# Optimization experiments

Measured on AMD Instinct MI355X. Metric: run time of the kernel, lower is better.

The kernel has to match this reference:

```python
import jax, jax.numpy as jnp
import numpy as np

B, T, C = 4, 2048, 1024
NUM_EXPERTS = 8
TOP_K = 2
D_EXPERT = 4 * C * TOP_K // NUM_EXPERTS  # 1024


def setup_inputs() -> dict:
    key = jax.random.key(0)
    k0, k1, k2, k3 = jax.random.split(key, 4)
    x = jax.random.normal(k0, (B, T, C), dtype=jnp.float32)
    # nn.Linear(n_embd, num_experts, bias=False).weight has shape [E, C]
    router_w = jax.random.normal(k1, (NUM_EXPERTS, C), dtype=jnp.float32) * 0.02
    # w1_all = stack of c_fc.weight.T  -> [E, C, D]
    w1_all = jax.random.normal(k2, (NUM_EXPERTS, C, D_EXPERT), dtype=jnp.float32) * 0.02
    # w2_all = stack of c_proj.weight.T -> [E, D, C]
    w2_all = jax.random.normal(k3, (NUM_EXPERTS, D_EXPERT, C), dtype=jnp.float32) * 0.02
    return {"x": x, "router_w": router_w, "w1_all": w1_all, "w2_all": w2_all}


def reference(x, router_w, w1_all, w2_all):
    b, t, c = x.shape
    x_flat = x.reshape(-1, c)                      # [N, C]
    router_logits = x_flat @ router_w.T            # [N, E]
    top_k_logits, top_k_idx = jax.lax.top_k(router_logits, TOP_K)  # [N, K]
    router_probs = jax.nn.softmax(top_k_logits, axis=-1)           # [N, K]

    # Same math as the original per-token weight gather, but computed as
    # dense all-expert GEMMs followed by an output gather (avoids the
    # [N, K, C, D] materialized weight copies while producing identical values).
    hidden = jnp.einsum('nc,ecd->ned', x_flat, w1_all)   # [N, E, D]
    hidden = jnp.square(jax.nn.relu(hidden))             # relu^2
    out_all = jnp.einsum('ned,edc->nec', hidden, w2_all) # [N, E, C]

    sel = jnp.take_along_axis(out_all, top_k_idx[:, :, None], axis=1)  # [N, K, C]
    out = jnp.sum(sel * router_probs[:, :, None], axis=1)             # [N, C]
    return out.reshape(b, t, c)
```

## Files before the change

### kernel.cpp

```cpp
#include <hip/hip_runtime.h>
#include <cstdint>
#include <cstddef>

typedef unsigned short ushort_t;
typedef unsigned short ushort8 __attribute__((ext_vector_type(8)));
typedef __bf16 bf16x8 __attribute__((ext_vector_type(8)));
typedef float floatx4 __attribute__((ext_vector_type(4)));

#define N_TOK 8192
#define CDIM 1024
#define NEXP 8

__device__ __forceinline__ float bf2f(ushort_t h) {
  union { unsigned int u; float f; } v; v.u = ((unsigned int)h) << 16; return v.f;
}
__device__ __forceinline__ ushort_t f2bf(float f) {
  union { float f; unsigned int u; } v; v.f = f;
  unsigned int r = v.u + 0x7fffu + ((v.u >> 16) & 1u);
  return (ushort_t)(r >> 16);
}

__device__ __forceinline__ void async_copy16(const ushort_t* g, ushort_t* l) {
  __builtin_amdgcn_global_load_lds(
      (const __attribute__((address_space(1))) unsigned int*)g,
      (__attribute__((address_space(3))) unsigned int*)l, 16, 0, 0);
}

__global__ void detect_init_kernel(const ushort_t* __restrict__ x,
                                   int* __restrict__ flag,
                                   int* __restrict__ cnt) {
  int tid = threadIdx.x;
  ushort_t u = x[tid];
  int ex = (u >> 7) & 0xFF;
  int crazy = (ex >= 0xC0 || ex <= 0x30) ? 1 : 0;
  int total = __syncthreads_count(crazy);
  if (tid == 0) flag[0] = (total >= 16) ? 1 : 0;
  if (tid < NEXP) cnt[tid] = 0;
}

__global__ void convert_x_kernel(const void* __restrict__ xv,
                                 const int* __restrict__ flag,
                                 ushort_t* __restrict__ xbf) {
  int idx = (blockIdx.x * 256 + threadIdx.x) * 8;
  if (flag[0]) {
    const float* xp = (const float*)xv + idx;
    floatx4 f0 = *(const floatx4*)xp;
    floatx4 f1 = *(const floatx4*)(xp + 4);
    ushort8 o;
#pragma unroll
    for (int i = 0; i < 4; i++) { o[i] = f2bf(f0[i]); o[4 + i] = f2bf(f1[i]); }
    *(ushort8*)(xbf + idx) = o;
  } else {
    *(ushort8*)(xbf + idx) = *(const ushort8*)((const ushort_t*)xv + idx);
  }
}

__global__ void router_compute(const void* __restrict__ xv,
                               const void* __restrict__ rwv,
                               const int* __restrict__ flag,
                               int* __restrict__ tok_e,
                               float* __restrict__ prob) {
  int isf32 = flag[0];
  int wid = threadIdx.x >> 6;
  int lane = threadIdx.x & 63;
  int t = blockIdx.x * 4 + wid;

  float acc[NEXP];
#pragma unroll
  for (int e = 0; e < NEXP; e++) acc[e] = 0.f;

  if (isf32) {
    const float* xr = (const float*)xv + (size_t)t * CDIM;
    const float* rw = (const float*)rwv;
#pragma unroll
    for (int half = 0; half < 2; half++) {
      int base = (lane + half * 64) * 8;
      floatx4 x0 = *(const floatx4*)(xr + base);
      floatx4 x1 = *(const floatx4*)(xr + base + 4);
#pragma unroll
      for (int e = 0; e < NEXP; e++) {
        floatx4 w0 = *(const floatx4*)(rw + e * CDIM + base);
        floatx4 w1 = *(const floatx4*)(rw + e * CDIM + base + 4);
        acc[e] += x0[0]*w0[0] + x0[1]*w0[1] + x0[2]*w0[2] + x0[3]*w0[3]
                + x1[0]*w1[0] + x1[1]*w1[1] + x1[2]*w1[2] + x1[3]*w1[3];
      }
    }
  } else {
    const ushort_t* xr = (const ushort_t*)xv + (size_t)t * CDIM;
    const ushort_t* rw = (const ushort_t*)rwv;
#pragma unroll
    for (int half = 0; half < 2; half++) {
      int base = (lane + half * 64) * 8;
      ushort8 xu = *(const ushort8*)(xr + base);
#pragma unroll
      for (int e = 0; e < NEXP; e++) {
        ushort8 wu = *(const ushort8*)(rw + e * CDIM + base);
#pragma unroll
        for (int i = 0; i < 8; i++) acc[e] += bf2f(xu[i]) * bf2f(wu[i]);
      }
    }
  }

#pragma unroll
  for (int e = 0; e < NEXP; e++) {
#pragma unroll
    for (int off = 32; off > 0; off >>= 1) acc[e] += __shfl_xor(acc[e], off);
  }

  if (lane == 0) {
    int e0 = 0; float l0 = acc[0];
#pragma unroll
    for (int e = 1; e < NEXP; e++) if (acc[e] > l0) { l0 = acc[e]; e0 = e; }
    int e1 = (e0 == 0) ? 1 : 0; float l1 = acc[e1];
#pragma unroll
    for (int e = 0; e < NEXP; e++) {
      if (e != e0 && acc[e] > l1) { l1 = acc[e]; e1 = e; }
    }
    float p0 = 1.f / (1.f + __expf(l1 - l0));
    tok_e[t] = e0 | (e1 << 8);
    prob[t * 2] = p0;
    prob[t * 2 + 1] = 1.f - p0;
  }
}

__global__ void scatter_kernel(const int* __restrict__ tok_e,
                               int* __restrict__ cnt,
                               int* __restrict__ slots) {
  __shared__ int lcnt[NEXP];
  __shared__ int gbase[NEXP];
  int tid = threadIdx.x;
  if (tid < NEXP) lcnt[tid] = 0;
  __syncthreads();
  int t = blockIdx.x * 1024 + tid;
  int ee = tok_e[t];
  int e0 = ee & 0xFF, e1 = (ee >> 8) & 0xFF;
  int lofs0 = atomicAdd(&lcnt[e0], 1);
  int lofs1 = atomicAdd(&lcnt[e1], 1);
  __syncthreads();
  if (tid < NEXP) gbase[tid] = atomicAdd(&cnt[tid], lcnt[tid]);
  __syncthreads();
  slots[e0 * N_TOK + gbase[e0] + lofs0] = t * 2;
  slots[e1 * N_TOK + gbase[e1] + lofs1] = t * 2 + 1;
}

__global__ void transpose_kernel(const void* __restrict__ w1v,
                                 const void* __restrict__ w2v,
                                 const int* __restrict__ flag,
                                 ushort_t* __restrict__ w1T,
                                 ushort_t* __restrict__ w2T) {
  int isf32 = flag[0];
  int z = blockIdx.z;
  size_t moff = (size_t)(z & 7) << 20;
  const void* srcv = (z < 8) ? w1v : w2v;
  ushort_t* dst = ((z < 8) ? w1T : w2T) + moff;

  __shared__ __align__(16) ushort_t tile[64][72];
  int t = threadIdx.x;
  int R0 = blockIdx.y * 64, C0 = blockIdx.x * 64;
  int r = t >> 2, cb = (t & 3) * 16;
  if (isf32) {
    const float* sp = (const float*)srcv + moff + (size_t)(R0 + r) * 1024 + C0 + cb;
    ushort8 o0, o1;
#pragma unroll
    for (int q = 0; q < 2; q++) {
      floatx4 f = *(const floatx4*)(sp + q * 4);
#pragma unroll
      for (int i = 0; i < 4; i++) o0[q * 4 + i] = f2bf(f[i]);
    }
#pragma unroll
    for (int q = 0; q < 2; q++) {
      floatx4 f = *(const floatx4*)(sp + 8 + q * 4);
#pragma unroll
      for (int i = 0; i < 4; i++) o1[q * 4 + i] = f2bf(f[i]);
    }
    *(ushort8*)&tile[r][cb] = o0;
    *(ushort8*)&tile[r][cb + 8] = o1;
  } else {
    const ushort_t* sp = (const ushort_t*)srcv + moff + (size_t)(R0 + r) * 1024 + C0 + cb;
    *(ushort8*)&tile[r][cb] = *(const ushort8*)sp;
    *(ushort8*)&tile[r][cb + 8] = *(const ushort8*)(sp + 8);
  }
  __syncthreads();
  int d = t >> 2, rb = (t & 3) * 16;
  ushort8 o0, o1;
#pragma unroll
  for (int j = 0; j < 8; j++) { o0[j] = tile[rb + j][d]; o1[j] = tile[rb + 8 + j][d]; }
  ushort_t* dp = dst + (size_t)(C0 + d) * 1024 + R0 + rb;
  *(ushort8*)dp = o0;
  *(ushort8*)(dp + 8) = o1;
}

template <int MODE>
__global__ __launch_bounds__(256) void moe_gemm(const ushort_t* __restrict__ A,
                                                const ushort_t* __restrict__ BT,
                                                ushort_t* __restrict__ Out,
                                                const int* __restrict__ cnt,
                                                const int* __restrict__ slots,
                                                const float* __restrict__ prob) {
  int e = blockIdx.z;
  int M = cnt[e];
  M = (M > N_TOK) ? N_TOK : M;
  int m0 = blockIdx.y * 128;
  if (m0 >= M) return;
  int n0 = blockIdx.x * 128;

  __shared__ __align__(16) ushort_t As[128 * 64];
  __shared__ __align__(16) ushort_t Bs[128 * 64];
  __shared__ int srow[128];

  int tid = threadIdx.x;
  if (tid < 128) {
    int gm = m0 + tid;
    int gi = (gm < M) ? gm : (M - 1);
    srow[tid] = slots[e * N_TOK + gi] & (2 * N_TOK - 1);
  }
  __syncthreads();

  int wid = tid >> 6;
  int lane = tid & 63;
  int lrow = lane >> 3;
  int gchunk = (lane & 7) ^ lrow;

  const ushort_t* aptr[4];
  const ushort_t* bptr[4];
  int rowbase = wid * 32;
#pragma unroll
  for (int j = 0; j < 4; j++) {
    int rr = rowbase + j * 8 + lrow;
    int s = srow[rr];
    int aidx = (MODE == 0) ? (s >> 1) : s;
    aptr[j] = A + (size_t)aidx * CDIM + gchunk * 8;
    bptr[j] = BT + ((size_t)e << 20) + (size_t)(n0 + rr) * 1024 + gchunk * 8;
  }
  ushort_t* albase = &As[rowbase * 64];
  ushort_t* blbase = &Bs[rowbase * 64];

  int wm = (wid >> 1) * 64;
  int wn = (wid & 1) * 64;
  int qd = lane >> 4;
  int ln = lane & 15;
  int l7 = ln & 7;

  floatx4 zero = {0.f, 0.f, 0.f, 0.f};
  floatx4 acc[4][4];
#pragma unroll
  for (int i = 0; i < 4; i++)
#pragma unroll
    for (int j = 0; j < 4; j++) acc[i][j] = zero;

  for (int k0 = 0; k0 < 1024; k0 += 64) {
    __syncthreads();
#pragma unroll
    for (int j = 0; j < 4; j++) {
      async_copy16(aptr[j] + k0, albase + j * 512);
      async_copy16(bptr[j] + k0, blbase + j * 512);
    }
    __syncthreads();
#pragma unroll
    for (int ks = 0; ks < 2; ks++) {
      bf16x8 afr[4], bfr[4];
#pragma unroll
      for (int i = 0; i < 4; i++) {
        int pc = ((ks * 4 + qd) ^ l7) * 8;
        afr[i] = *(const bf16x8*)&As[(wm + i * 16 + ln) * 64 + pc];
        bfr[i] = *(const bf16x8*)&Bs[(wn + i * 16 + ln) * 64 + pc];
      }
#pragma unroll
      for (int i = 0; i < 4; i++)
#pragma unroll
        for (int j = 0; j < 4; j++)
          acc[i][j] = __builtin_amdgcn_mfma_f32_16x16x32_bf16(afr[i], bfr[j], acc[i][j], 0, 0, 0);
    }
  }

#pragma unroll
  for (int i = 0; i < 4; i++) {
#pragma unroll
    for (int r = 0; r < 4; r++) {
      int rl = wm + i * 16 + qd * 4 + r;
      int gm = m0 + rl;
      if (gm >= M) continue;
      int s = srow[rl];
      float p = (MODE == 1) ? prob[s] : 0.f;
      ushort_t* orow = Out + (size_t)s * 1024 + n0 + wn + ln;
#pragma unroll
      for (int j = 0; j < 4; j++) {
        float v = acc[i][j][r];
        if (MODE == 0) { v = fmaxf(v, 0.f); v = v * v; }
        else v *= p;
        orow[j * 16] = f2bf(v);
      }
    }
  }
}

__global__ void combine_kernel(const ushort_t* __restrict__ oslots,
                               float* __restrict__ out) {
  int idx = (blockIdx.x * 256 + threadIdx.x) * 8;
  int t = idx >> 10;
  int c = idx & 1023;
  const ushort_t* r0 = oslots + ((size_t)t * 2) * 1024 + c;
  const ushort_t* r1 = r0 + 1024;
  ushort8 a = *(const ushort8*)r0;
  ushort8 b = *(const ushort8*)r1;
  floatx4 o0, o1;
#pragma unroll
  for (int i = 0; i < 4; i++) o0[i] = bf2f(a[i]) + bf2f(b[i]);
#pragma unroll
  for (int i = 0; i < 4; i++) o1[i] = bf2f(a[4 + i]) + bf2f(b[4 + i]);
  *(floatx4*)(out + idx) = o0;
  *(floatx4*)(out + idx + 4) = o1;
}

extern "C" void kernel_launch(void* const* d_in, const int* in_sizes, int n_in,
                              void* d_out, int out_size, void* d_ws, size_t ws_size,
                              hipStream_t stream) {
  const void* x  = d_in[0];
  const void* rw = d_in[1];
  const void* w1 = d_in[2];
  const void* w2 = d_in[3];
  float* out = (float*)d_out;
  char* ws = (char*)d_ws;

  int* cnt  = (int*)(ws + 0);
  int* flag = (int*)(ws + 64);
  int* slots = (int*)(ws + 1024);
  float* prob = (float*)(ws + 263168);
  int* tok_e = (int*)(ws + 335872);
  ushort_t* xbf = (ushort_t*)(ws + 524288);
  ushort_t* w1T = (ushort_t*)(ws + 17301504);
  ushort_t* hidden = (ushort_t*)(ws + 34078720);
  ushort_t* w2T = (ushort_t*)(ws + 67633152);
  ushort_t* oslots = (ushort_t*)(ws + 524288);

  detect_init_kernel<<<1, 128, 0, stream>>>((const ushort_t*)x, flag, cnt);
  router_compute<<<N_TOK / 4, 256, 0, stream>>>(x, rw, flag, tok_e, prob);
  scatter_kernel<<<NEXP, 1024, 0, stream>>>(tok_e, cnt, slots);
  convert_x_kernel<<<4096, 256, 0, stream>>>(x, flag, xbf);
  transpose_kernel<<<dim3(16, 16, 16), 256, 0, stream>>>(w1, w2, flag, w1T, w2T);
  moe_gemm<0><<<dim3(8, 64, 8), 256, 0, stream>>>(xbf, w1T, hidden, cnt, slots, prob);
  moe_gemm<1><<<dim3(8, 64, 8), 256, 0, stream>>>(hidden, w2T, oslots, cnt, slots, prob);
  combine_kernel<<<4096, 256, 0, stream>>>(oslots, out);
}
```

Before: 302.1 us.

## Fuse x bf16 conversion into router, enlarge GEMM M-tile to 256 with 512 threads

The separate convert_x kernel is removed and the bf16 copy of x is written from inside router_compute, which already reads x, saving one launch and one full read of x. The MoE GEMM now uses 256x128 tiles with 512 threads and a flattened 1D grid ordered expert-fastest, so each B tile is reused across twice as many rows and B loads per thread are halved. The larger LDS footprint and higher thread count may lower occupancy, and coarser M tiles waste more work on partially filled expert tails.

```diff
diff --git a/kernel.cpp b/kernel.cpp
--- a/kernel.cpp
+++ b/kernel.cpp
@@ -38,28 +38,12 @@
   if (tid < NEXP) cnt[tid] = 0;
 }
 
-__global__ void convert_x_kernel(const void* __restrict__ xv,
-                                 const int* __restrict__ flag,
-                                 ushort_t* __restrict__ xbf) {
-  int idx = (blockIdx.x * 256 + threadIdx.x) * 8;
-  if (flag[0]) {
-    const float* xp = (const float*)xv + idx;
-    floatx4 f0 = *(const floatx4*)xp;
-    floatx4 f1 = *(const floatx4*)(xp + 4);
-    ushort8 o;
-#pragma unroll
-    for (int i = 0; i < 4; i++) { o[i] = f2bf(f0[i]); o[4 + i] = f2bf(f1[i]); }
-    *(ushort8*)(xbf + idx) = o;
-  } else {
-    *(ushort8*)(xbf + idx) = *(const ushort8*)((const ushort_t*)xv + idx);
-  }
-}
-
 __global__ void router_compute(const void* __restrict__ xv,
                                const void* __restrict__ rwv,
                                const int* __restrict__ flag,
                                int* __restrict__ tok_e,
-                               float* __restrict__ prob) {
+                               float* __restrict__ prob,
+                               ushort_t* __restrict__ xbf) {
   int isf32 = flag[0];
   int wid = threadIdx.x >> 6;
   int lane = threadIdx.x & 63;
@@ -77,6 +61,10 @@
       int base = (lane + half * 64) * 8;
       floatx4 x0 = *(const floatx4*)(xr + base);
       floatx4 x1 = *(const floatx4*)(xr + base + 4);
+      ushort8 o;
+#pragma unroll
+      for (int i = 0; i < 4; i++) { o[i] = f2bf(x0[i]); o[4 + i] = f2bf(x1[i]); }
+      *(ushort8*)(xbf + (size_t)t * CDIM + base) = o;
 #pragma unroll
       for (int e = 0; e < NEXP; e++) {
         floatx4 w0 = *(const floatx4*)(rw + e * CDIM + base);
@@ -92,6 +80,7 @@
     for (int half = 0; half < 2; half++) {
       int base = (lane + half * 64) * 8;
       ushort8 xu = *(const ushort8*)(xr + base);
+      *(ushort8*)(xbf + (size_t)t * CDIM + base) = xu;
 #pragma unroll
       for (int e = 0; e < NEXP; e++) {
         ushort8 wu = *(const ushort8*)(rw + e * CDIM + base);
@@ -191,25 +180,28 @@
 }
 
 template <int MODE>
-__global__ __launch_bounds__(256) void moe_gemm(const ushort_t* __restrict__ A,
-                                                const ushort_t* __restrict__ BT,
-                                                ushort_t* __restrict__ Out,
-                                                const int* __restrict__ cnt,
-                                                const int* __restrict__ slots,
-                                                const float* __restrict__ prob) {
-  int e = blockIdx.z;
+__global__ __launch_bounds__(512, 4) void moe_gemm(const ushort_t* __restrict__ A,
+                                                   const ushort_t* __restrict__ BT,
+                                                   ushort_t* __restrict__ Out,
+                                                   const int* __restrict__ cnt,
+                                                   const int* __restrict__ slots,
+                                                   const float* __restrict__ prob) {
+  int bid = blockIdx.x;
+  int e = bid & 7;
+  int nt = (bid >> 3) & 7;
+  int mt = bid >> 6;
   int M = cnt[e];
   M = (M > N_TOK) ? N_TOK : M;
-  int m0 = blockIdx.y * 128;
+  int m0 = mt * 256;
   if (m0 >= M) return;
-  int n0 = blockIdx.x * 128;
-
-  __shared__ __align__(16) ushort_t As[128 * 64];
+  int n0 = nt * 128;
+
+  __shared__ __align__(16) ushort_t As[256 * 64];
   __shared__ __align__(16) ushort_t Bs[128 * 64];
-  __shared__ int srow[128];
+  __shared__ int srow[256];
 
   int tid = threadIdx.x;
-  if (tid < 128) {
+  if (tid < 256) {
     int gm = m0 + tid;
     int gi = (gm < M) ? gm : (M - 1);
     srow[tid] = slots[e * N_TOK + gi] & (2 * N_TOK - 1);
@@ -222,18 +214,23 @@
   int gchunk = (lane & 7) ^ lrow;
 
   const ushort_t* aptr[4];
-  const ushort_t* bptr[4];
-  int rowbase = wid * 32;
+  const ushort_t* bptr[2];
+  int arowbase = wid * 32;
+  int browbase = wid * 16;
 #pragma unroll
   for (int j = 0; j < 4; j++) {
-    int rr = rowbase + j * 8 + lrow;
+    int rr = arowbase + j * 8 + lrow;
     int s = srow[rr];
     int aidx = (MODE == 0) ? (s >> 1) : s;
     aptr[j] = A + (size_t)aidx * CDIM + gchunk * 8;
+  }
+#pragma unroll
+  for (int j = 0; j < 2; j++) {
+    int rr = browbase + j * 8 + lrow;
     bptr[j] = BT + ((size_t)e << 20) + (size_t)(n0 + rr) * 1024 + gchunk * 8;
   }
-  ushort_t* albase = &As[rowbase * 64];
-  ushort_t* blbase = &Bs[rowbase * 64];
+  ushort_t* albase = &As[arowbase * 64];
+  ushort_t* blbase = &Bs[browbase * 64];
 
   int wm = (wid >> 1) * 64;
   int wn = (wid & 1) * 64;
@@ -251,10 +248,9 @@
   for (int k0 = 0; k0 < 1024; k0 += 64) {
     __syncthreads();
 #pragma unroll
-    for (int j = 0; j < 4; j++) {
-      async_copy16(aptr[j] + k0, albase + j * 512);
-      async_copy16(bptr[j] + k0, blbase + j * 512);
-    }
+    for (int j = 0; j < 4; j++) async_copy16(aptr[j] + k0, albase + j * 512);
+#pragma unroll
+    for (int j = 0; j < 2; j++) async_copy16(bptr[j] + k0, blbase + j * 512);
     __syncthreads();
 #pragma unroll
     for (int ks = 0; ks < 2; ks++) {
@@ -334,11 +330,10 @@
   ushort_t* oslots = (ushort_t*)(ws + 524288);
 
   detect_init_kernel<<<1, 128, 0, stream>>>((const ushort_t*)x, flag, cnt);
-  router_compute<<<N_TOK / 4, 256, 0, stream>>>(x, rw, flag, tok_e, prob);
+  router_compute<<<N_TOK / 4, 256, 0, stream>>>(x, rw, flag, tok_e, prob, xbf);
   scatter_kernel<<<NEXP, 1024, 0, stream>>>(tok_e, cnt, slots);
-  convert_x_kernel<<<4096, 256, 0, stream>>>(x, flag, xbf);
   transpose_kernel<<<dim3(16, 16, 16), 256, 0, stream>>>(w1, w2, flag, w1T, w2T);
-  moe_gemm<0><<<dim3(8, 64, 8), 256, 0, stream>>>(xbf, w1T, hidden, cnt, slots, prob);
-  moe_gemm<1><<<dim3(8, 64, 8), 256, 0, stream>>>(hidden, w2T, oslots, cnt, slots, prob);
+  moe_gemm<0><<<2048, 512, 0, stream>>>(xbf, w1T, hidden, cnt, slots, prob);
+  moe_gemm<1><<<2048, 512, 0, stream>>>(hidden, w2T, oslots, cnt, slots, prob);
   combine_kernel<<<4096, 256, 0, stream>>>(oslots, out);
 }
```

Measured after the change: 274.3 us. 1.1x faster.
